# Performance work log

Hardware: AMD Instinct MI355X
Metric: run time of the kernel (lower is better)

Reference implementation:

```python
import jax, jax.numpy as jnp
import numpy as np
import math

HEAD_DIM = 128
THETA = 10000.0
MASK_VAL = -10000.0


def _rope(x, cos, sin):
    # x: (B, S, D); cos/sin: (S, D//2). Pairs (even, odd) rotated as complex.
    xr = x.reshape(*x.shape[:-1], -1, 2)
    xe, xo = xr[..., 0], xr[..., 1]
    oe = xe * cos - xo * sin
    oo = xe * sin + xo * cos
    return jnp.stack([oe, oo], axis=-1).reshape(x.shape)


def setup_inputs() -> dict:
    key = jax.random.key(0)
    B, S, D = 8, 4096, HEAD_DIM
    qkv = jax.random.normal(key, (B, S, 3 * D), dtype=jnp.float32)
    return {"qkv": qkv}


def reference(qkv):
    B, S, threeD = qkv.shape
    D = threeD // 3
    qkv = qkv.reshape(B, S, 3, D)
    q, k, v = qkv[:, :, 0], qkv[:, :, 1], qkv[:, :, 2]

    # precompute_freqs_cis: outer(t, 1/theta^(2i/d)) -> cos/sin (S, D//2)
    inv_freq = 1.0 / (THETA ** (jnp.arange(0, D, 2, dtype=jnp.float32) / D))
    freqs = jnp.arange(S, dtype=jnp.float32)[:, None] * inv_freq[None, :]
    cos, sin = jnp.cos(freqs), jnp.sin(freqs)
    q = _rope(q, cos, sin)
    k = _rope(k, cos, sin)

    scale = 1.0 / math.sqrt(D)
    scores = jnp.einsum('btd,bsd->bts', q, k) * scale  # (B, S, S)
    causal_mask = jnp.triu(jnp.full((S, S), MASK_VAL, dtype=scores.dtype), 1)
    attn = jax.nn.softmax(scores + causal_mask, axis=-1)
    out = jnp.einsum('bts,bsd->btd', attn, v)  # (B, S, D)
    return out
```

## Files before the change

### kernel.cpp

```cpp
#include <hip/hip_runtime.h>
#include <math.h>

typedef _Float16 half8 __attribute__((ext_vector_type(8)));
typedef float floatx4 __attribute__((ext_vector_type(4)));
typedef float floatx2 __attribute__((ext_vector_type(2)));

#define B_ 8
#define S_ 4096
#define SCALE_L2E 0.12751743008389106f
#define MASK_L2E  -14426.950408889634f
#define L2_10K_OVER_128 0.10381025296522975f

#define PLD2 40
#define KW  136
#define VW  24
#define OSTLD 136
#define SLOTS_PER_B 576
#define NW 8
#define KVBUF 8192
#define NBUF 3
#define POFF (NBUF * KVBUF)
#define POOL_HALFS (POFF + NW * 2 * 16 * PLD2)

__device__ __forceinline__ int chunk_prefix(int qt32) {
    int g = qt32 >> 4;
    return qt32 + 8 * g * (g - 1) + (qt32 - (g << 4)) * g;
}

__device__ __forceinline__ void glds16(const _Float16* src, _Float16* dst) {
    __builtin_amdgcn_global_load_lds((const __attribute__((address_space(1))) void*)src,
                                     (__attribute__((address_space(3))) void*)dst, 16, 0, 0);
}

__global__ __launch_bounds__(256) void prep_kernel(const float* __restrict__ qkv,
                                                   _Float16* __restrict__ Qh,
                                                   _Float16* __restrict__ Kp,
                                                   _Float16* __restrict__ Vp) {
    __shared__ __align__(16) _Float16 Kl[16][KW];
    __shared__ __align__(16) _Float16 Vt[128][VW];
    const int tid = threadIdx.x;
    const int b   = blockIdx.y;
    const int s0  = blockIdx.x * 16;

#pragma unroll
    for (int it = 0; it < 4; ++it) {
        int idx = tid + it * 256;
        int i = idx & 63, sr = idx >> 6, s = s0 + sr;
        const float* base = qkv + ((size_t)(b * S_ + s)) * 384 + 2 * i;
        floatx2 q2 = *(const floatx2*)base;
        floatx2 k2 = *(const floatx2*)(base + 128);
        float inv = exp2f(-(float)(2 * i) * L2_10K_OVER_128);
        float ang = (float)s * inv;
        float sn, cs;
        __sincosf(ang, &sn, &cs);
        size_t oq = ((size_t)(b * S_ + s)) * 128 + 2 * i;
        Qh[oq]     = (_Float16)((q2[0] * cs - q2[1] * sn) * SCALE_L2E);
        Qh[oq + 1] = (_Float16)((q2[0] * sn + q2[1] * cs) * SCALE_L2E);
        Kl[sr][2 * i]     = (_Float16)(k2[0] * cs - k2[1] * sn);
        Kl[sr][2 * i + 1] = (_Float16)(k2[0] * sn + k2[1] * cs);
    }
#pragma unroll
    for (int it = 0; it < 2; ++it) {
        int idx = tid + it * 256;
        int c = idx & 31, sr = idx >> 5;
        floatx4 v = *(const floatx4*)(qkv + ((size_t)(b * S_ + s0 + sr)) * 384 + 256 + c * 4);
#pragma unroll
        for (int j = 0; j < 4; ++j) Vt[c * 4 + j][sr] = (_Float16)v[j];
    }
    __syncthreads();

    {
        int c = tid >> 6, lane = tid & 63;
        int quad = lane >> 4, n = lane & 15;
        half8 val = *(const half8*)&Kl[n][c * 32 + quad * 8];
        int s16 = s0 >> 4;
        *(half8*)(Kp + (((size_t)(b * 256 + s16) * 4 + c) * 64 + lane) * 8) = val;
    }
    {
        int kt = s0 >> 6, c2 = (s0 >> 5) & 1, qp = (s0 >> 4) & 1;
        int nt = tid >> 5, lq = (tid >> 4) & 1, n = tid & 15;
        int quad = qp * 2 + lq;
        int lane = quad * 16 + n;
        half8 val = *(const half8*)&Vt[nt * 16 + n][lq * 8];
        *(half8*)(Vp + ((((size_t)(b * 64 + kt) * 2 + c2) * 8 + nt) * 64 + lane) * 8) = val;
    }
}

__global__ __launch_bounds__(512) void attn_part_kernel(const _Float16* __restrict__ Qh,
                                                        const _Float16* __restrict__ Kp,
                                                        const _Float16* __restrict__ Vp,
                                                        _Float16* __restrict__ Ppart,
                                                        float* __restrict__ Lpart) {
    __shared__ __align__(16) _Float16 POOL[POOL_HALFS];

    const int tid  = threadIdx.x;
    const int w    = tid >> 6;
    const int lane = tid & 63;
    const int quad = lane >> 4;
    const int l16  = lane & 15;
    const int b     = blockIdx.x & 7;
    const int chunk = blockIdx.x >> 3;
    const int c0    = chunk * 8;

    const int qt32_top  = 127 - blockIdx.y * 8;
    const int ktmax_blk = (qt32_top * 32 + 31) >> 6;
    if (c0 > ktmax_blk) return;
    const int kend_blk  = min(ktmax_blk, c0 + 7);

    const int qt32   = qt32_top - w;
    const int qr0    = qt32 * 32;
    const int kt_max = (qr0 + 31) >> 6;
    const bool has_work = (c0 <= kt_max);
    const int kend   = min(kt_max, c0 + 7);
    const int slot   = b * SLOTS_PER_B + chunk_prefix(qt32) + chunk;
    _Float16* Pw = POOL + POFF + w * (2 * 16 * PLD2);

    half8 aq[2][4];
#pragma unroll
    for (int tile = 0; tile < 2; ++tile) {
        const _Float16* Qb = Qh + ((size_t)(b * S_) + qr0 + tile * 16 + l16) * 128;
#pragma unroll
        for (int c = 0; c < 4; ++c) aq[tile][c] = *(const half8*)(Qb + c * 32 + quad * 8);
    }

    floatx4 o[2][8];
#pragma unroll
    for (int tile = 0; tile < 2; ++tile)
#pragma unroll
        for (int i = 0; i < 8; ++i) o[tile][i] = (floatx4){0.f, 0.f, 0.f, 0.f};
    float rsum[2][4] = {{0.f, 0.f, 0.f, 0.f}, {0.f, 0.f, 0.f, 0.f}};

    const _Float16* Kb = Kp + (size_t)b * 524288;
    const _Float16* Vb = Vp + (size_t)b * 524288;

    const int ht0    = 2 * c0;
    const int ht_end = 2 * kend_blk + 1;

#define STAGE(ht_)                                                                \
    do {                                                                          \
        const _Float16* ks_ = Kb + (size_t)(ht_) * 4096 + w * 512 + lane * 8;     \
        const _Float16* vs_ = Vb + (size_t)(ht_) * 4096 + w * 512 + lane * 8;     \
        _Float16* d_ = POOL + ((ht_) % NBUF) * KVBUF + w * 512;                   \
        glds16(ks_, d_);                                                          \
        glds16(vs_, d_ + 4096);                                                   \
    } while (0)

    STAGE(ht0);
    STAGE(ht0 + 1);

    for (int ht = ht0; ht <= ht_end; ++ht) {
        if (ht < ht_end) {
            asm volatile("s_waitcnt vmcnt(2)" ::: "memory");
        } else {
            asm volatile("s_waitcnt vmcnt(0)" ::: "memory");
        }
        __builtin_amdgcn_s_barrier();
        if (ht + 2 <= ht_end) STAGE(ht + 2);

        const int kt = ht >> 1, h = ht & 1;
        if (has_work && kt <= kend) {
            const _Float16* Klds = POOL + (ht % NBUF) * KVBUF;
            const _Float16* Vlds = Klds + 4096;

            floatx4 s4[2][2];
#pragma unroll
            for (int tl = 0; tl < 2; ++tl) {
                half8 bk[4];
#pragma unroll
                for (int c = 0; c < 4; ++c)
                    bk[c] = *(const half8*)&Klds[((tl * 4 + c) * 64 + lane) * 8];
                floatx4 a0 = (floatx4){0.f, 0.f, 0.f, 0.f};
                floatx4 a1 = (floatx4){0.f, 0.f, 0.f, 0.f};
#pragma unroll
                for (int c = 0; c < 4; ++c) {
                    a0 = __builtin_amdgcn_mfma_f32_16x16x32_f16(aq[0][c], bk[c], a0, 0, 0, 0);
                    a1 = __builtin_amdgcn_mfma_f32_16x16x32_f16(aq[1][c], bk[c], a1, 0, 0, 0);
                }
                s4[0][tl] = a0; s4[1][tl] = a1;
            }

            half8 vf[8];
#pragma unroll
            for (int nt = 0; nt < 8; ++nt)
                vf[nt] = *(const half8*)&Vlds[(nt * 64 + lane) * 8];

            if (kt == kt_max) {
#pragma unroll
                for (int tile = 0; tile < 2; ++tile)
#pragma unroll
                    for (int tl = 0; tl < 2; ++tl)
#pragma unroll
                        for (int r = 0; r < 4; ++r) {
                            int kcol = kt * 64 + h * 32 + tl * 16 + l16;
                            int qr   = qr0 + tile * 16 + quad * 4 + r;
                            if (kcol > qr) s4[tile][tl][r] += MASK_L2E;
                        }
            }

#pragma unroll
            for (int tile = 0; tile < 2; ++tile)
#pragma unroll
                for (int tl = 0; tl < 2; ++tl)
#pragma unroll
                    for (int r = 0; r < 4; ++r) {
                        float p = __builtin_amdgcn_exp2f(s4[tile][tl][r]);
                        rsum[tile][r] += p;
                        Pw[tile * (16 * PLD2) + (quad * 4 + r) * PLD2 + tl * 16 + l16] = (_Float16)p;
                    }

#pragma unroll
            for (int tile = 0; tile < 2; ++tile) {
                half8 ap = *(const half8*)&Pw[tile * (16 * PLD2) + l16 * PLD2 + quad * 8];
#pragma unroll
                for (int nt = 0; nt < 8; ++nt)
                    o[tile][nt] = __builtin_amdgcn_mfma_f32_16x16x32_f16(ap, vf[nt], o[tile][nt], 0, 0, 0);
            }
        }
    }
#undef STAGE

    __builtin_amdgcn_s_barrier();

    if (!has_work) return;

#pragma unroll
    for (int off = 1; off <= 8; off <<= 1)
#pragma unroll
        for (int tile = 0; tile < 2; ++tile)
#pragma unroll
            for (int r = 0; r < 4; ++r)
                rsum[tile][r] += __shfl_xor(rsum[tile][r], off, 64);
    if (l16 == 0) {
#pragma unroll
        for (int tile = 0; tile < 2; ++tile)
#pragma unroll
            for (int r = 0; r < 4; ++r)
                Lpart[(size_t)slot * 32 + tile * 16 + quad * 4 + r] = rsum[tile][r];
    }

    _Float16* Ost = POOL + w * (POOL_HALFS / NW);
    _Float16* pp = Ppart + (size_t)slot * 4096;
#pragma unroll
    for (int tile = 0; tile < 2; ++tile) {
#pragma unroll
        for (int nt = 0; nt < 8; ++nt)
#pragma unroll
            for (int r = 0; r < 4; ++r)
                Ost[(quad * 4 + r) * OSTLD + nt * 16 + l16] = (_Float16)o[tile][nt][r];
#pragma unroll
        for (int i = 0; i < 4; ++i) {
            int idx = lane + i * 64;
            half8 v = *(const half8*)&Ost[(idx >> 4) * OSTLD + (idx & 15) * 8];
            *(half8*)(pp + ((size_t)tile * 256 + idx) * 8) = v;
        }
    }
}

__global__ __launch_bounds__(256) void reduce_kernel(const _Float16* __restrict__ Ppart,
                                                     const float* __restrict__ Lpart,
                                                     float* __restrict__ out) {
    const int bid  = blockIdx.x;
    const int b    = bid >> 7;
    const int qt32 = bid & 127;
    const int qr0  = qt32 * 32;
    const int nch  = (((qr0 + 31) >> 6) >> 3) + 1;
    const int slot0 = b * SLOTS_PER_B + chunk_prefix(qt32);
    const _Float16* pp = Ppart + (size_t)slot0 * 4096;
    const float* lp = Lpart + (size_t)slot0 * 32;
    const int tid = threadIdx.x;

#pragma unroll
    for (int j = 0; j < 2; ++j) {
        int idx = tid + j * 256;
        int row = idx >> 4;
        float acc[8] = {0.f, 0.f, 0.f, 0.f, 0.f, 0.f, 0.f, 0.f};
        float l = 0.f;
        for (int c = 0; c < nch; ++c) {
            half8 v = *(const half8*)(pp + (size_t)c * 4096 + (size_t)idx * 8);
#pragma unroll
            for (int k = 0; k < 8; ++k) acc[k] += (float)v[k];
            l += lp[c * 32 + row];
        }
        float inv = 1.0f / l;
        float* ob = out + ((size_t)(b * S_) + qr0) * 128 + (size_t)idx * 8;
        floatx4 o0 = (floatx4){acc[0] * inv, acc[1] * inv, acc[2] * inv, acc[3] * inv};
        floatx4 o1 = (floatx4){acc[4] * inv, acc[5] * inv, acc[6] * inv, acc[7] * inv};
        *(floatx4*)ob = o0;
        *(floatx4*)(ob + 4) = o1;
    }
}

#define PLD 72
__global__ __launch_bounds__(64) void attn_atomic_kernel(const _Float16* __restrict__ Qh,
                                                         const _Float16* __restrict__ Kp,
                                                         const _Float16* __restrict__ Vp,
                                                         float* __restrict__ out,
                                                         float* __restrict__ Lg) {
    __shared__ __align__(16) _Float16 Pl[2][16 * PLD];
    const int lane = threadIdx.x, quad = lane >> 4, l16 = lane & 15;
    const int b = blockIdx.x & 7, chunk = blockIdx.x >> 3;
    const int qt = 255 - blockIdx.y, qr0 = qt * 16;
    const int kt_max = qt >> 2, c0 = chunk * 8;
    if (c0 > kt_max) return;
    const int kend = min(kt_max, c0 + 7);
    const _Float16* Qb = Qh + ((size_t)(b * S_) + qr0 + l16) * 128;
    half8 aq[4];
#pragma unroll
    for (int c = 0; c < 4; ++c) aq[c] = *(const half8*)(Qb + c * 32 + quad * 8);
    floatx4 o[8];
#pragma unroll
    for (int i = 0; i < 8; ++i) o[i] = (floatx4){0.f, 0.f, 0.f, 0.f};
    float rsum[4] = {0.f, 0.f, 0.f, 0.f};
    const _Float16* Kb = Kp + (size_t)b * 524288;
    const _Float16* Vb = Vp + (size_t)b * 524288;
    for (int kt = c0; kt <= kend; ++kt) {
        half8 vf[2][8];
#pragma unroll
        for (int c2 = 0; c2 < 2; ++c2)
#pragma unroll
            for (int nt = 0; nt < 8; ++nt)
                vf[c2][nt] = *(const half8*)(Vb + (((size_t)(kt * 2 + c2) * 8 + nt) * 64 + lane) * 8);
        floatx4 s4[4];
#pragma unroll
        for (int t = 0; t < 4; ++t) {
            const _Float16* kp = Kb + ((size_t)((kt * 4 + t) * 4) * 64 + lane) * 8;
            floatx4 acc = (floatx4){0.f, 0.f, 0.f, 0.f};
#pragma unroll
            for (int c = 0; c < 4; ++c) {
                half8 bk = *(const half8*)(kp + c * 512);
                acc = __builtin_amdgcn_mfma_f32_16x16x32_f16(aq[c], bk, acc, 0, 0, 0);
            }
            s4[t] = acc;
        }
        if (kt == kt_max) {
#pragma unroll
            for (int t = 0; t < 4; ++t)
#pragma unroll
                for (int r = 0; r < 4; ++r) {
                    int kcol = kt * 64 + t * 16 + l16;
                    int qr = qr0 + quad * 4 + r;
                    if (kcol > qr) s4[t][r] += MASK_L2E;
                }
        }
        const int buf = kt & 1;
#pragma unroll
        for (int t = 0; t < 4; ++t)
#pragma unroll
            for (int r = 0; r < 4; ++r) {
                float p = __builtin_amdgcn_exp2f(s4[t][r]);
                rsum[r] += p;
                Pl[buf][(quad * 4 + r) * PLD + t * 16 + l16] = (_Float16)p;
            }
#pragma unroll
        for (int c2 = 0; c2 < 2; ++c2) {
            half8 ap = *(const half8*)&Pl[buf][l16 * PLD + c2 * 32 + quad * 8];
#pragma unroll
            for (int nt = 0; nt < 8; ++nt)
                o[nt] = __builtin_amdgcn_mfma_f32_16x16x32_f16(ap, vf[c2][nt], o[nt], 0, 0, 0);
        }
    }
#pragma unroll
    for (int off = 1; off <= 8; off <<= 1)
#pragma unroll
        for (int r = 0; r < 4; ++r)
            rsum[r] += __shfl_xor(rsum[r], off, 64);
    if (l16 == 0) {
#pragma unroll
        for (int r = 0; r < 4; ++r)
            atomicAdd(&Lg[(size_t)(b * S_) + qr0 + quad * 4 + r], rsum[r]);
    }
    float* ob = out + ((size_t)(b * S_) + qr0) * 128;
#pragma unroll
    for (int nt = 0; nt < 8; ++nt)
#pragma unroll
        for (int r = 0; r < 4; ++r)
            atomicAdd(&ob[(quad * 4 + r) * 128 + nt * 16 + l16], o[nt][r]);
}

__global__ __launch_bounds__(256) void norm_kernel(float* __restrict__ out,
                                                   const float* __restrict__ Lg) {
    int i = blockIdx.x * 256 + threadIdx.x;
    int row = i >> 5;
    floatx4 v = *(floatx4*)(out + (size_t)i * 4);
    float inv = 1.0f / Lg[row];
    v[0] *= inv; v[1] *= inv; v[2] *= inv; v[3] *= inv;
    *(floatx4*)(out + (size_t)i * 4) = v;
}

extern "C" void kernel_launch(void* const* d_in, const int* in_sizes, int n_in,
                              void* d_out, int out_size, void* d_ws, size_t ws_size,
                              hipStream_t stream) {
    const float* qkv = (const float*)d_in[0];
    float* out = (float*)d_out;
    const size_t MB = 1024 * 1024;
    _Float16* Qh = (_Float16*)d_ws;
    _Float16* Kp = (_Float16*)((char*)d_ws + 8 * MB);
    _Float16* Vp = (_Float16*)((char*)d_ws + 16 * MB);

    const size_t lpart_bytes = (size_t)B_ * SLOTS_PER_B * 32 * sizeof(float);
    const size_t ppart_bytes = (size_t)B_ * SLOTS_PER_B * 4096 * sizeof(_Float16);
    const size_t need = 25 * MB + ppart_bytes;

    prep_kernel<<<dim3(256, B_), dim3(256), 0, stream>>>(qkv, Qh, Kp, Vp);

    if (ws_size >= need) {
        float*    Lpart = (float*)((char*)d_ws + 24 * MB);
        _Float16* Ppart = (_Float16*)((char*)d_ws + 25 * MB);
        (void)lpart_bytes;
        attn_part_kernel<<<dim3(64, 16), dim3(512), 0, stream>>>(Qh, Kp, Vp, Ppart, Lpart);
        reduce_kernel<<<dim3(1024), dim3(256), 0, stream>>>(Ppart, Lpart, out);
    } else {
        float* Lg = (float*)((char*)d_ws + 24 * MB);
        hipMemsetAsync(out, 0, (size_t)B_ * S_ * 128 * sizeof(float), stream);
        hipMemsetAsync(Lg, 0, (size_t)B_ * S_ * sizeof(float), stream);
        attn_atomic_kernel<<<dim3(64, 256), dim3(64), 0, stream>>>(Qh, Kp, Vp, out, Lg);
        norm_kernel<<<dim3(4096), dim3(256), 0, stream>>>(out, Lg);
    }
}
```

Measured before the change: 165.0 us.

## Switch attention to 32x32x16 MFMA and keep P in registers via permlane swap

Rewrites the main attention kernel to use 32x32x16 MFMA tiles, computing S^T = K·Q so the exponentiated scores can be repacked into the A-operand layout with v_permlane32_swap instead of a round trip through LDS. The K/V prepacking in the prep kernel is changed to the new fragment layout, and the old layout is kept in a legacy prep kernel for the atomic fallback path. This removes the per-tile LDS write and read of P and lowers instruction count per MFMA. The cost is larger accumulator register usage and a dependence on gfx950-specific permlane instructions.

```diff
diff --git a/kernel.cpp b/kernel.cpp
--- a/kernel.cpp
+++ b/kernel.cpp
@@ -3,6 +3,7 @@
 
 typedef _Float16 half8 __attribute__((ext_vector_type(8)));
 typedef float floatx4 __attribute__((ext_vector_type(4)));
+typedef float floatx16 __attribute__((ext_vector_type(16)));
 typedef float floatx2 __attribute__((ext_vector_type(2)));
 
 #define B_ 8
@@ -11,7 +12,6 @@
 #define MASK_L2E  -14426.950408889634f
 #define L2_10K_OVER_128 0.10381025296522975f
 
-#define PLD2 40
 #define KW  136
 #define VW  24
 #define OSTLD 136
@@ -19,8 +19,7 @@
 #define NW 8
 #define KVBUF 8192
 #define NBUF 3
-#define POFF (NBUF * KVBUF)
-#define POOL_HALFS (POFF + NW * 2 * 16 * PLD2)
+#define POOL_HALFS (NBUF * KVBUF)
 
 __device__ __forceinline__ int chunk_prefix(int qt32) {
     int g = qt32 >> 4;
@@ -30,6 +29,12 @@
 __device__ __forceinline__ void glds16(const _Float16* src, _Float16* dst) {
     __builtin_amdgcn_global_load_lds((const __attribute__((address_space(1))) void*)src,
                                      (__attribute__((address_space(3))) void*)dst, 16, 0, 0);
+}
+
+__device__ __forceinline__ unsigned pack2(float a, float b) {
+    union { _Float16 h[2]; unsigned u; } x;
+    x.h[0] = (_Float16)a; x.h[1] = (_Float16)b;
+    return x.u;
 }
 
 __global__ __launch_bounds__(256) void prep_kernel(const float* __restrict__ qkv,
@@ -69,20 +74,20 @@
     }
     __syncthreads();
 
+    const int ht = s0 >> 5;
     {
-        int c = tid >> 6, lane = tid & 63;
-        int quad = lane >> 4, n = lane & 15;
-        half8 val = *(const half8*)&Kl[n][c * 32 + quad * 8];
-        int s16 = s0 >> 4;
-        *(half8*)(Kp + (((size_t)(b * 256 + s16) * 4 + c) * 64 + lane) * 8) = val;
+        int g = tid >> 4, sr = tid & 15;
+        int r = s0 + sr;
+        int c = g >> 1, dh = g & 1;
+        int l = (r & 31) + (dh << 5);
+        half8 val = *(const half8*)&Kl[sr][g * 8];
+        *(half8*)(Kp + (((size_t)(b * 128 + ht) * 8 + c) * 64 + l) * 8) = val;
     }
     {
-        int kt = s0 >> 6, c2 = (s0 >> 5) & 1, qp = (s0 >> 4) & 1;
-        int nt = tid >> 5, lq = (tid >> 4) & 1, n = tid & 15;
-        int quad = qp * 2 + lq;
-        int lane = quad * 16 + n;
-        half8 val = *(const half8*)&Vt[nt * 16 + n][lq * 8];
-        *(half8*)(Vp + ((((size_t)(b * 64 + kt) * 2 + c2) * 8 + nt) * 64 + lane) * 8) = val;
+        int n = tid >> 6, l = tid & 63;
+        int sh = (s0 >> 4) & 1;
+        half8 val = *(const half8*)&Vt[n * 32 + (l & 31)][(l >> 5) * 8];
+        *(half8*)(Vp + (((size_t)(b * 128 + ht) * 8 + sh * 4 + n) * 64 + l) * 8) = val;
     }
 }
 
@@ -96,8 +101,8 @@
     const int tid  = threadIdx.x;
     const int w    = tid >> 6;
     const int lane = tid & 63;
-    const int quad = lane >> 4;
-    const int l16  = lane & 15;
+    const int l31  = lane & 31;
+    const int lh   = lane >> 5;
     const int b     = blockIdx.x & 7;
     const int chunk = blockIdx.x >> 3;
     const int c0    = chunk * 8;
@@ -113,22 +118,20 @@
     const bool has_work = (c0 <= kt_max);
     const int kend   = min(kt_max, c0 + 7);
     const int slot   = b * SLOTS_PER_B + chunk_prefix(qt32) + chunk;
-    _Float16* Pw = POOL + POFF + w * (2 * 16 * PLD2);
-
-    half8 aq[2][4];
-#pragma unroll
-    for (int tile = 0; tile < 2; ++tile) {
-        const _Float16* Qb = Qh + ((size_t)(b * S_) + qr0 + tile * 16 + l16) * 128;
-#pragma unroll
-        for (int c = 0; c < 4; ++c) aq[tile][c] = *(const half8*)(Qb + c * 32 + quad * 8);
-    }
-
-    floatx4 o[2][8];
-#pragma unroll
-    for (int tile = 0; tile < 2; ++tile)
-#pragma unroll
-        for (int i = 0; i < 8; ++i) o[tile][i] = (floatx4){0.f, 0.f, 0.f, 0.f};
-    float rsum[2][4] = {{0.f, 0.f, 0.f, 0.f}, {0.f, 0.f, 0.f, 0.f}};
+
+    half8 aq[8];
+    {
+        const _Float16* Qb = Qh + ((size_t)(b * S_) + qr0 + l31) * 128 + lh * 8;
+#pragma unroll
+        for (int c = 0; c < 8; ++c) aq[c] = *(const half8*)(Qb + c * 16);
+    }
+
+    floatx16 o[4];
+#pragma unroll
+    for (int n = 0; n < 4; ++n)
+#pragma unroll
+        for (int r = 0; r < 16; ++r) o[n][r] = 0.f;
+    float rsum = 0.f;
 
     const _Float16* Kb = Kp + (size_t)b * 524288;
     const _Float16* Vb = Vp + (size_t)b * 524288;
@@ -157,64 +160,57 @@
         __builtin_amdgcn_s_barrier();
         if (ht + 2 <= ht_end) STAGE(ht + 2);
 
-        const int kt = ht >> 1, h = ht & 1;
+        const int kt = ht >> 1;
         if (has_work && kt <= kend) {
             const _Float16* Klds = POOL + (ht % NBUF) * KVBUF;
             const _Float16* Vlds = Klds + 4096;
 
-            floatx4 s4[2][2];
-#pragma unroll
-            for (int tl = 0; tl < 2; ++tl) {
-                half8 bk[4];
-#pragma unroll
-                for (int c = 0; c < 4; ++c)
-                    bk[c] = *(const half8*)&Klds[((tl * 4 + c) * 64 + lane) * 8];
-                floatx4 a0 = (floatx4){0.f, 0.f, 0.f, 0.f};
-                floatx4 a1 = (floatx4){0.f, 0.f, 0.f, 0.f};
-#pragma unroll
-                for (int c = 0; c < 4; ++c) {
-                    a0 = __builtin_amdgcn_mfma_f32_16x16x32_f16(aq[0][c], bk[c], a0, 0, 0, 0);
-                    a1 = __builtin_amdgcn_mfma_f32_16x16x32_f16(aq[1][c], bk[c], a1, 0, 0, 0);
+            floatx16 Cs;
+#pragma unroll
+            for (int r = 0; r < 16; ++r) Cs[r] = 0.f;
+#pragma unroll
+            for (int c = 0; c < 8; ++c) {
+                half8 ak = *(const half8*)&Klds[(c * 64 + lane) * 8];
+                Cs = __builtin_amdgcn_mfma_f32_32x32x16_f16(ak, aq[c], Cs, 0, 0, 0);
+            }
+
+            half8 bv[8];
+#pragma unroll
+            for (int i = 0; i < 8; ++i)
+                bv[i] = *(const half8*)&Vlds[(i * 64 + lane) * 8];
+
+            if (kt == kt_max) {
+#pragma unroll
+                for (int r = 0; r < 16; ++r) {
+                    int kl = (r & 3) + 8 * (r >> 2) + 4 * lh;
+                    if (ht * 32 + kl > qr0 + l31) Cs[r] += MASK_L2E;
                 }
-                s4[0][tl] = a0; s4[1][tl] = a1;
-            }
-
-            half8 vf[8];
-#pragma unroll
-            for (int nt = 0; nt < 8; ++nt)
-                vf[nt] = *(const half8*)&Vlds[(nt * 64 + lane) * 8];
-
-            if (kt == kt_max) {
-#pragma unroll
-                for (int tile = 0; tile < 2; ++tile)
-#pragma unroll
-                    for (int tl = 0; tl < 2; ++tl)
-#pragma unroll
-                        for (int r = 0; r < 4; ++r) {
-                            int kcol = kt * 64 + h * 32 + tl * 16 + l16;
-                            int qr   = qr0 + tile * 16 + quad * 4 + r;
-                            if (kcol > qr) s4[tile][tl][r] += MASK_L2E;
-                        }
-            }
-
-#pragma unroll
-            for (int tile = 0; tile < 2; ++tile)
-#pragma unroll
-                for (int tl = 0; tl < 2; ++tl)
-#pragma unroll
-                    for (int r = 0; r < 4; ++r) {
-                        float p = __builtin_amdgcn_exp2f(s4[tile][tl][r]);
-                        rsum[tile][r] += p;
-                        Pw[tile * (16 * PLD2) + (quad * 4 + r) * PLD2 + tl * 16 + l16] = (_Float16)p;
-                    }
-
-#pragma unroll
-            for (int tile = 0; tile < 2; ++tile) {
-                half8 ap = *(const half8*)&Pw[tile * (16 * PLD2) + l16 * PLD2 + quad * 8];
-#pragma unroll
-                for (int nt = 0; nt < 8; ++nt)
-                    o[tile][nt] = __builtin_amdgcn_mfma_f32_16x16x32_f16(ap, vf[nt], o[tile][nt], 0, 0, 0);
-            }
+            }
+
+            float e[16];
+#pragma unroll
+            for (int r = 0; r < 16; ++r) {
+                e[r] = __builtin_amdgcn_exp2f(Cs[r]);
+                rsum += e[r];
+            }
+            unsigned A0 = pack2(e[0], e[1]),  B0 = pack2(e[2], e[3]);
+            unsigned C0 = pack2(e[4], e[5]),  D0 = pack2(e[6], e[7]);
+            unsigned A1 = pack2(e[8], e[9]),  B1 = pack2(e[10], e[11]);
+            unsigned C1 = pack2(e[12], e[13]), D1 = pack2(e[14], e[15]);
+            asm("v_permlane32_swap_b32 %0, %1" : "+v"(A0), "+v"(C0));
+            asm("v_permlane32_swap_b32 %0, %1" : "+v"(B0), "+v"(D0));
+            asm("v_permlane32_swap_b32 %0, %1" : "+v"(A1), "+v"(C1));
+            asm("v_permlane32_swap_b32 %0, %1" : "+v"(B1), "+v"(D1));
+            union { unsigned u[4]; half8 v; } pa0, pa1;
+            pa0.u[0] = A0; pa0.u[1] = B0; pa0.u[2] = C0; pa0.u[3] = D0;
+            pa1.u[0] = A1; pa1.u[1] = B1; pa1.u[2] = C1; pa1.u[3] = D1;
+
+#pragma unroll
+            for (int n = 0; n < 4; ++n)
+                o[n] = __builtin_amdgcn_mfma_f32_32x32x16_f16(pa0.v, bv[n], o[n], 0, 0, 0);
+#pragma unroll
+            for (int n = 0; n < 4; ++n)
+                o[n] = __builtin_amdgcn_mfma_f32_32x32x16_f16(pa1.v, bv[4 + n], o[n], 0, 0, 0);
         }
     }
 #undef STAGE
@@ -223,35 +219,25 @@
 
     if (!has_work) return;
 
-#pragma unroll
-    for (int off = 1; off <= 8; off <<= 1)
-#pragma unroll
-        for (int tile = 0; tile < 2; ++tile)
-#pragma unroll
-            for (int r = 0; r < 4; ++r)
-                rsum[tile][r] += __shfl_xor(rsum[tile][r], off, 64);
-    if (l16 == 0) {
-#pragma unroll
-        for (int tile = 0; tile < 2; ++tile)
-#pragma unroll
-            for (int r = 0; r < 4; ++r)
-                Lpart[(size_t)slot * 32 + tile * 16 + quad * 4 + r] = rsum[tile][r];
-    }
-
-    _Float16* Ost = POOL + w * (POOL_HALFS / NW);
+    rsum += __shfl_xor(rsum, 32, 64);
+    if (lane < 32) Lpart[(size_t)slot * 32 + lane] = rsum;
+
+    _Float16* Ost = POOL + w * 3072;
     _Float16* pp = Ppart + (size_t)slot * 4096;
 #pragma unroll
-    for (int tile = 0; tile < 2; ++tile) {
-#pragma unroll
-        for (int nt = 0; nt < 8; ++nt)
-#pragma unroll
-            for (int r = 0; r < 4; ++r)
-                Ost[(quad * 4 + r) * OSTLD + nt * 16 + l16] = (_Float16)o[tile][nt][r];
+    for (int t = 0; t < 2; ++t) {
+#pragma unroll
+        for (int n = 0; n < 4; ++n)
+#pragma unroll
+            for (int rr = 0; rr < 8; ++rr) {
+                int row = (rr & 3) + 8 * (rr >> 2) + 4 * lh;
+                Ost[row * OSTLD + n * 32 + l31] = (_Float16)o[n][t * 8 + rr];
+            }
 #pragma unroll
         for (int i = 0; i < 4; ++i) {
             int idx = lane + i * 64;
             half8 v = *(const half8*)&Ost[(idx >> 4) * OSTLD + (idx & 15) * 8];
-            *(half8*)(pp + ((size_t)tile * 256 + idx) * 8) = v;
+            *(half8*)(pp + ((size_t)t * 2048 + (size_t)idx * 8)) = v;
         }
     }
 }
@@ -291,6 +277,58 @@
 }
 
 #define PLD 72
+__global__ __launch_bounds__(256) void prep_legacy_kernel(const float* __restrict__ qkv,
+                                                          _Float16* __restrict__ Qh,
+                                                          _Float16* __restrict__ Kp,
+                                                          _Float16* __restrict__ Vp) {
+    __shared__ __align__(16) _Float16 Kl[16][KW];
+    __shared__ __align__(16) _Float16 Vt[128][VW];
+    const int tid = threadIdx.x;
+    const int b   = blockIdx.y;
+    const int s0  = blockIdx.x * 16;
+#pragma unroll
+    for (int it = 0; it < 4; ++it) {
+        int idx = tid + it * 256;
+        int i = idx & 63, sr = idx >> 6, s = s0 + sr;
+        const float* base = qkv + ((size_t)(b * S_ + s)) * 384 + 2 * i;
+        floatx2 q2 = *(const floatx2*)base;
+        floatx2 k2 = *(const floatx2*)(base + 128);
+        float inv = exp2f(-(float)(2 * i) * L2_10K_OVER_128);
+        float ang = (float)s * inv;
+        float sn, cs;
+        __sincosf(ang, &sn, &cs);
+        size_t oq = ((size_t)(b * S_ + s)) * 128 + 2 * i;
+        Qh[oq]     = (_Float16)((q2[0] * cs - q2[1] * sn) * SCALE_L2E);
+        Qh[oq + 1] = (_Float16)((q2[0] * sn + q2[1] * cs) * SCALE_L2E);
+        Kl[sr][2 * i]     = (_Float16)(k2[0] * cs - k2[1] * sn);
+        Kl[sr][2 * i + 1] = (_Float16)(k2[0] * sn + k2[1] * cs);
+    }
+#pragma unroll
+    for (int it = 0; it < 2; ++it) {
+        int idx = tid + it * 256;
+        int c = idx & 31, sr = idx >> 5;
+        floatx4 v = *(const floatx4*)(qkv + ((size_t)(b * S_ + s0 + sr)) * 384 + 256 + c * 4);
+#pragma unroll
+        for (int j = 0; j < 4; ++j) Vt[c * 4 + j][sr] = (_Float16)v[j];
+    }
+    __syncthreads();
+    {
+        int c = tid >> 6, lane = tid & 63;
+        int quad = lane >> 4, n = lane & 15;
+        half8 val = *(const half8*)&Kl[n][c * 32 + quad * 8];
+        int s16 = s0 >> 4;
+        *(half8*)(Kp + (((size_t)(b * 256 + s16) * 4 + c) * 64 + lane) * 8) = val;
+    }
+    {
+        int kt = s0 >> 6, c2 = (s0 >> 5) & 1, qp = (s0 >> 4) & 1;
+        int nt = tid >> 5, lq = (tid >> 4) & 1, n = tid & 15;
+        int quad = qp * 2 + lq;
+        int lane = quad * 16 + n;
+        half8 val = *(const half8*)&Vt[nt * 16 + n][lq * 8];
+        *(half8*)(Vp + ((((size_t)(b * 64 + kt) * 2 + c2) * 8 + nt) * 64 + lane) * 8) = val;
+    }
+}
+
 __global__ __launch_bounds__(64) void attn_atomic_kernel(const _Float16* __restrict__ Qh,
                                                          const _Float16* __restrict__ Kp,
                                                          const _Float16* __restrict__ Vp,
@@ -397,19 +435,17 @@
     _Float16* Kp = (_Float16*)((char*)d_ws + 8 * MB);
     _Float16* Vp = (_Float16*)((char*)d_ws + 16 * MB);
 
-    const size_t lpart_bytes = (size_t)B_ * SLOTS_PER_B * 32 * sizeof(float);
     const size_t ppart_bytes = (size_t)B_ * SLOTS_PER_B * 4096 * sizeof(_Float16);
     const size_t need = 25 * MB + ppart_bytes;
-
-    prep_kernel<<<dim3(256, B_), dim3(256), 0, stream>>>(qkv, Qh, Kp, Vp);
 
     if (ws_size >= need) {
         float*    Lpart = (float*)((char*)d_ws + 24 * MB);
         _Float16* Ppart = (_Float16*)((char*)d_ws + 25 * MB);
-        (void)lpart_bytes;
+        prep_kernel<<<dim3(256, B_), dim3(256), 0, stream>>>(qkv, Qh, Kp, Vp);
         attn_part_kernel<<<dim3(64, 16), dim3(512), 0, stream>>>(Qh, Kp, Vp, Ppart, Lpart);
         reduce_kernel<<<dim3(1024), dim3(256), 0, stream>>>(Ppart, Lpart, out);
     } else {
+        prep_legacy_kernel<<<dim3(256, B_), dim3(256), 0, stream>>>(qkv, Qh, Kp, Vp);
         float* Lg = (float*)((char*)d_ws + 24 * MB);
         hipMemsetAsync(out, 0, (size_t)B_ * S_ * 128 * sizeof(float), stream);
         hipMemsetAsync(Lg, 0, (size_t)B_ * S_ * sizeof(float), stream);
```

Result: faster. 152.5 us (-7.6%).
